# Kernel optimization log

Measured on AMD Instinct MI355X. Metric: run time of the kernel, lower is better.

## Reference

```python
import jax, jax.numpy as jnp
import numpy as np
import math

B, S, D, H = 2, 2048, 1024, 16
HD = D // H  # 64


def _rope(x, cos, sin):
    # x: [B,S,H,HD]; cos/sin: [S, HD//2]
    x2 = x.reshape(*x.shape[:-1], HD // 2, 2)
    x0, x1 = x2[..., 0], x2[..., 1]
    c = cos[None, :, None, :]
    s = sin[None, :, None, :]
    r0 = x0 * c - x1 * s
    r1 = x0 * s + x1 * c
    return jnp.stack([r0, r1], axis=-1).reshape(x.shape)


def setup_inputs() -> dict:
    key = jax.random.key(0)
    ks = jax.random.split(key, 6)
    x = jax.random.normal(ks[0], (B, S, D), dtype=jnp.float32)
    wq = jax.random.normal(ks[1], (D, D), dtype=jnp.float32) * 0.02
    wk = jax.random.normal(ks[2], (D, D), dtype=jnp.float32) * 0.02
    wv = jax.random.normal(ks[3], (D, D), dtype=jnp.float32) * 0.02
    wo = jax.random.normal(ks[4], (D, D), dtype=jnp.float32) * 0.02
    # standard RoPE frequencies: theta = 10000^(-2i/HD)
    inv_freq = 1.0 / (10000.0 ** (jnp.arange(0, HD, 2, dtype=jnp.float32) / HD))
    t = jnp.arange(S, dtype=jnp.float32)
    ang = t[:, None] * inv_freq[None, :]  # [S, HD//2]
    freqs_cos = jnp.cos(ang)
    freqs_sin = jnp.sin(ang)
    # causal additive mask [S, S]
    mask = jnp.where(jnp.tril(jnp.ones((S, S), dtype=bool)), 0.0, -1e9).astype(jnp.float32)
    return {"x": x, "wq": wq, "wk": wk, "wv": wv, "wo": wo,
            "freqs_cos": freqs_cos, "freqs_sin": freqs_sin, "mask": mask}


def reference(x, wq, wk, wv, wo, freqs_cos, freqs_sin, mask):
    b, s, d = x.shape
    # nn.Linear with no bias: y = x @ W^T
    q = jnp.einsum('bsd,od->bso', x, wq).reshape(b, s, H, HD)
    k = jnp.einsum('bsd,od->bso', x, wk).reshape(b, s, H, HD)
    v = jnp.einsum('bsd,od->bso', x, wv).reshape(b, s, H, HD)
    q = _rope(q, freqs_cos, freqs_sin)
    k = _rope(k, freqs_cos, freqs_sin)
    # [B,H,S,HD]
    q = q.transpose(0, 2, 1, 3)
    k = k.transpose(0, 2, 1, 3)
    v = v.transpose(0, 2, 1, 3)
    scores = jnp.einsum('bhqd,bhkd->bhqk', q, k) / math.sqrt(HD)
    scores = scores + mask[None, None, :, :]
    p = jax.nn.softmax(scores.astype(jnp.float32), axis=-1).astype(q.dtype)
    out = jnp.einsum('bhqk,bhkd->bhqd', p, v)
    out = out.transpose(0, 2, 1, 3).reshape(b, s, d)
    return jnp.einsum('bsd,od->bso', out, wo)
```

## Files before the change

kernel.cpp:

```cpp
#include <hip/hip_runtime.h>
#include <hip/hip_bf16.h>
#include <stdint.h>

#define NB 2
#define NS 2048
#define ND 1024
#define NH 16
#define NM (NB*NS)

typedef __attribute__((ext_vector_type(8))) short bf16x8;
typedef __attribute__((ext_vector_type(4))) float f32x4;

static __device__ __forceinline__ f32x4 mfma16(bf16x8 a, bf16x8 b, f32x4 c) {
  return __builtin_amdgcn_mfma_f32_16x16x32_bf16(a, b, c, 0, 0, 0);
}

static __device__ __forceinline__ void gload_lds16(const void* g, void* l) {
  __builtin_amdgcn_global_load_lds(
      (const __attribute__((address_space(1))) void*)g,
      (__attribute__((address_space(3))) void*)l, 16, 0, 0);
}

static __device__ __forceinline__ uint32_t pkbf2(float a, float b) {
  return (uint32_t)__bfloat16_as_ushort(__float2bfloat16(a)) |
         ((uint32_t)__bfloat16_as_ushort(__float2bfloat16(b)) << 16);
}

struct alignas(8) bh4 { __hip_bfloat16 x, y, z, w; };

__global__ void cvt_bf16(const float* __restrict__ in,
                         __hip_bfloat16* __restrict__ out, int n4) {
  int i = blockIdx.x * blockDim.x + threadIdx.x;
  int stride = gridDim.x * blockDim.x;
  for (; i < n4; i += stride) {
    float4 v = reinterpret_cast<const float4*>(in)[i];
    bh4 o;
    o.x = __float2bfloat16(v.x);
    o.y = __float2bfloat16(v.y);
    o.z = __float2bfloat16(v.z);
    o.w = __float2bfloat16(v.w);
    reinterpret_cast<bh4*>(out)[i] = o;
  }
}

__global__ void cvt_w4(const float* __restrict__ w0, const float* __restrict__ w1,
                       const float* __restrict__ w2, const float* __restrict__ w3,
                       __hip_bfloat16* o0, __hip_bfloat16* o1,
                       __hip_bfloat16* o2, __hip_bfloat16* o3) {
  const int t = blockIdx.x >> 10;
  const float* in = (t == 0) ? w0 : (t == 1) ? w1 : (t == 2) ? w2 : w3;
  __hip_bfloat16* out = (t == 0) ? o0 : (t == 1) ? o1 : (t == 2) ? o2 : o3;
  const int i = (blockIdx.x & 1023) * 256 + threadIdx.x;
  float4 v = reinterpret_cast<const float4*>(in)[i];
  bh4 o;
  o.x = __float2bfloat16(v.x);
  o.y = __float2bfloat16(v.y);
  o.z = __float2bfloat16(v.z);
  o.w = __float2bfloat16(v.w);
  reinterpret_cast<bh4*>(out)[i] = o;
}

template <int MODE>
__global__ __launch_bounds__(256) void gemm_proj(
    const __hip_bfloat16* __restrict__ A,
    const __hip_bfloat16* __restrict__ W,
    const float* __restrict__ fcos,
    const float* __restrict__ fsin,
    void* __restrict__ outp) {
  __shared__ __hip_bfloat16 sA[128 * 32];
  __shared__ __hip_bfloat16 sB[64 * 32];

  const int tid = threadIdx.x;
  const int wid = tid >> 6;
  const int lane = tid & 63;
  const int l4 = lane >> 4, l16 = lane & 15;
  const int brow = blockIdx.x * 128;
  const int bcol = blockIdx.y * 64;
  const int wr = (wid >> 1) * 64;
  const int wc = (wid & 1) * 32;

  f32x4 acc[4][2] = {};

  const __hip_bfloat16* Ap = A + (size_t)(brow + (tid >> 2)) * 1024 + (tid & 3) * 8;
  const __hip_bfloat16* Wp = W + (size_t)(bcol + (tid >> 2)) * 1024 + (tid & 3) * 8;
  char* sAc = (char*)sA + wid * 1024;
  char* sBc = (char*)sB + wid * 1024;

  for (int kt = 0; kt < 32; ++kt) {
    const int k0 = kt * 32;
    __syncthreads();
    gload_lds16(Ap + k0,             sAc);
    gload_lds16(Ap + 64 * 1024 + k0, sAc + 4096);
    gload_lds16(Wp + k0,             sBc);
    __syncthreads();

    bf16x8 af[4], bfr[2];
#pragma unroll
    for (int i = 0; i < 4; ++i)
      af[i] = *(const bf16x8*)&sA[(wr + i * 16 + l16) * 32 + l4 * 8];
#pragma unroll
    for (int i = 0; i < 2; ++i)
      bfr[i] = *(const bf16x8*)&sB[(wc + i * 16 + l16) * 32 + l4 * 8];
#pragma unroll
    for (int mi = 0; mi < 4; ++mi)
#pragma unroll
      for (int ni = 0; ni < 2; ++ni)
        acc[mi][ni] = mfma16(af[mi], bfr[ni], acc[mi][ni]);
  }

#pragma unroll
  for (int mi = 0; mi < 4; ++mi)
#pragma unroll
    for (int ni = 0; ni < 2; ++ni)
#pragma unroll
      for (int j = 0; j < 4; ++j) {
        float v = acc[mi][ni][j];
        const int row = brow + wr + mi * 16 + l4 * 4 + j;
        const int col = bcol + wc + ni * 16 + l16;
        if (MODE == 3) {
          ((float*)outp)[(size_t)row * 1024 + col] = v;
        } else if (MODE == 2) {
          const int bb = row >> 11, ss = row & 2047;
          const int hh = col >> 6, hd = col & 63;
          ((__hip_bfloat16*)outp)[((size_t)(bb * 16 + hh) * 64 + hd) * 2048 + ss] =
              __float2bfloat16(v);
        } else {
          float other = __shfl_xor(v, 1);
          const int ss = row & 2047;
          const int p = (col & 63) >> 1;
          const float c = fcos[ss * 32 + p];
          const float sn = fsin[ss * 32 + p];
          float r = (col & 1) ? (other * sn + v * c) : (v * c - other * sn);
          if (MODE == 0) r *= 0.125f;
          const int bb = row >> 11;
          const int hh = col >> 6, hd = col & 63;
          ((__hip_bfloat16*)outp)[((size_t)(bb * 16 + hh) * 2048 + ss) * 64 + hd] =
              __float2bfloat16(r);
        }
      }
}

__global__ __launch_bounds__(256) void attn_fwd(
    const __hip_bfloat16* __restrict__ Q,
    const __hip_bfloat16* __restrict__ K,
    const __hip_bfloat16* __restrict__ VT,
    __hip_bfloat16* __restrict__ AO) {
  const int L = blockIdx.x;
  int qt, bh;
  if (L < 256) { qt = 15 - (L >> 5); bh = L & 31; }
  else         { qt = (L >> 5) - 8;  bh = L & 31; }
  const int bb = bh >> 4;
  const int hh = bh & 15;
  const int tid = threadIdx.x;
  const int wid = tid >> 6;
  const int lane = tid & 63;
  const int l4 = lane >> 4, l16 = lane & 15;
  const int wq0 = qt * 128 + wid * 32;

  const __hip_bfloat16* Qg = Q + (size_t)bh * 2048 * 64;
  const __hip_bfloat16* Kg = K + (size_t)bh * 2048 * 64;
  const __hip_bfloat16* Vg = VT + (size_t)bh * 64 * 2048;

  __shared__ __hip_bfloat16 sK[2][64][72];
  __shared__ __hip_bfloat16 sV[2][64][72];
  __shared__ __hip_bfloat16 sP[4][32][72];

  bf16x8 qf[2][2];
#pragma unroll
  for (int q2 = 0; q2 < 2; ++q2)
#pragma unroll
    for (int dk = 0; dk < 2; ++dk)
      qf[q2][dk] = *(const bf16x8*)&Qg[(size_t)(wq0 + q2 * 16 + l16) * 64 + dk * 32 + l4 * 8];

  float mrun[2] = {-1e30f, -1e30f};
  float lrun[2] = {0.f, 0.f};
  f32x4 oacc[2][4] = {};

  const int sr = tid >> 3;
  const int so = (tid & 7) * 8;
  const int nkv = 2 * qt + 2;

  uint4 kreg[2], vreg[2];
#pragma unroll
  for (int i = 0; i < 2; ++i) {
    kreg[i] = *(const uint4*)&Kg[(size_t)(i * 32 + sr) * 64 + so];
    vreg[i] = *(const uint4*)&Vg[(size_t)(i * 32 + sr) * 2048 + so];
  }
#pragma unroll
  for (int i = 0; i < 2; ++i) {
    *(uint4*)&sK[0][i * 32 + sr][so] = kreg[i];
    *(uint4*)&sV[0][i * 32 + sr][so] = vreg[i];
  }
  __syncthreads();

  for (int kv = 0; kv < nkv; ++kv) {
    const int cur = kv & 1, nxt = cur ^ 1;
    const int kb = kv * 64;

    if (kv + 1 < nkv) {
      const int kb2 = kb + 64;
#pragma unroll
      for (int i = 0; i < 2; ++i) {
        kreg[i] = *(const uint4*)&Kg[(size_t)(kb2 + i * 32 + sr) * 64 + so];
        vreg[i] = *(const uint4*)&Vg[(size_t)(i * 32 + sr) * 2048 + kb2 + so];
      }
    }

    if (kb <= wq0 + 31) {
      f32x4 sacc[4][2] = {};
#pragma unroll
      for (int dk = 0; dk < 2; ++dk) {
        bf16x8 kfr[4];
#pragma unroll
        for (int kf = 0; kf < 4; ++kf)
          kfr[kf] = *(const bf16x8*)&sK[cur][kf * 16 + l16][dk * 32 + l4 * 8];
#pragma unroll
        for (int kf = 0; kf < 4; ++kf)
#pragma unroll
          for (int q2 = 0; q2 < 2; ++q2)
            sacc[kf][q2] = mfma16(kfr[kf], qf[q2][dk], sacc[kf][q2]);
      }

      const bool need_mask = (kb + 63 > wq0);
      float fac[2];
#pragma unroll
      for (int q2 = 0; q2 < 2; ++q2) {
        const int qi = wq0 + q2 * 16 + l16;
        float pv[16];
#pragma unroll
        for (int kf = 0; kf < 4; ++kf)
#pragma unroll
          for (int j = 0; j < 4; ++j) {
            float s = sacc[kf][q2][j];
            if (need_mask && (kb + kf * 16 + l4 * 4 + j > qi)) s = -1e30f;
            pv[kf * 4 + j] = s;
          }
        float m0 = fmaxf(fmaxf(pv[0], pv[1]), fmaxf(pv[2], pv[3]));
        float m1 = fmaxf(fmaxf(pv[4], pv[5]), fmaxf(pv[6], pv[7]));
        float m2 = fmaxf(fmaxf(pv[8], pv[9]), fmaxf(pv[10], pv[11]));
        float m3 = fmaxf(fmaxf(pv[12], pv[13]), fmaxf(pv[14], pv[15]));
        float mloc = fmaxf(fmaxf(m0, m1), fmaxf(m2, m3));
        mloc = fmaxf(mloc, __shfl_xor(mloc, 16));
        mloc = fmaxf(mloc, __shfl_xor(mloc, 32));
        const float mold = mrun[q2];
        const float mnew = fmaxf(mold, mloc);
        const float f = __expf(mold - mnew);
        fac[q2] = f;
        mrun[q2] = mnew;
        float ts = 0.f;
        float pe[16];
#pragma unroll
        for (int t = 0; t < 16; ++t) { pe[t] = __expf(pv[t] - mnew); ts += pe[t]; }
#pragma unroll
        for (int kf = 0; kf < 4; ++kf) {
          uint2 w;
          w.x = pkbf2(pe[kf * 4 + 0], pe[kf * 4 + 1]);
          w.y = pkbf2(pe[kf * 4 + 2], pe[kf * 4 + 3]);
          *(uint2*)&sP[wid][q2 * 16 + l16][kf * 16 + l4 * 4] = w;
        }
        ts += __shfl_xor(ts, 16);
        ts += __shfl_xor(ts, 32);
        lrun[q2] = lrun[q2] * f + ts;
      }

#pragma unroll
      for (int mf = 0; mf < 2; ++mf)
#pragma unroll
        for (int j = 0; j < 4; ++j) {
          const float fr = __shfl(fac[mf], l4 * 4 + j);
#pragma unroll
          for (int df = 0; df < 4; ++df) oacc[mf][df][j] *= fr;
        }

#pragma unroll
      for (int ks = 0; ks < 2; ++ks) {
        bf16x8 pfr[2], vfr[4];
#pragma unroll
        for (int mf = 0; mf < 2; ++mf)
          pfr[mf] = *(const bf16x8*)&sP[wid][mf * 16 + l16][ks * 32 + l4 * 8];
#pragma unroll
        for (int df = 0; df < 4; ++df)
          vfr[df] = *(const bf16x8*)&sV[cur][df * 16 + l16][ks * 32 + l4 * 8];
#pragma unroll
        for (int mf = 0; mf < 2; ++mf)
#pragma unroll
          for (int df = 0; df < 4; ++df)
            oacc[mf][df] = mfma16(pfr[mf], vfr[df], oacc[mf][df]);
      }
    }

    if (kv + 1 < nkv) {
#pragma unroll
      for (int i = 0; i < 2; ++i) {
        *(uint4*)&sK[nxt][i * 32 + sr][so] = kreg[i];
        *(uint4*)&sV[nxt][i * 32 + sr][so] = vreg[i];
      }
    }
    __syncthreads();
  }

  float inv[2];
#pragma unroll
  for (int q2 = 0; q2 < 2; ++q2) inv[q2] = 1.f / lrun[q2];
#pragma unroll
  for (int mf = 0; mf < 2; ++mf)
#pragma unroll
    for (int j = 0; j < 4; ++j) {
      const float ir = __shfl(inv[mf], l4 * 4 + j);
      const int ss = wq0 + mf * 16 + l4 * 4 + j;
#pragma unroll
      for (int df = 0; df < 4; ++df) {
        const int dd = hh * 64 + df * 16 + l16;
        AO[((size_t)bb * 2048 + ss) * 1024 + dd] =
            __float2bfloat16(oacc[mf][df][j] * ir);
      }
    }
}

extern "C" void kernel_launch(void* const* d_in, const int* in_sizes, int n_in,
                              void* d_out, int out_size, void* d_ws, size_t ws_size,
                              hipStream_t stream) {
  const float* x  = (const float*)d_in[0];
  const float* wq = (const float*)d_in[1];
  const float* wk = (const float*)d_in[2];
  const float* wv = (const float*)d_in[3];
  const float* wo = (const float*)d_in[4];
  const float* fc = (const float*)d_in[5];
  const float* fs = (const float*)d_in[6];

  char* ws = (char*)d_ws;
  const size_t MB = 1024 * 1024;
  __hip_bfloat16* xb  = (__hip_bfloat16*)(ws);
  __hip_bfloat16* wqb = (__hip_bfloat16*)(ws + 8 * MB);
  __hip_bfloat16* wkb = (__hip_bfloat16*)(ws + 10 * MB);
  __hip_bfloat16* wvb = (__hip_bfloat16*)(ws + 12 * MB);
  __hip_bfloat16* wob = (__hip_bfloat16*)(ws + 14 * MB);
  __hip_bfloat16* qws = (__hip_bfloat16*)(ws + 16 * MB);
  __hip_bfloat16* kws = (__hip_bfloat16*)(ws + 24 * MB);
  __hip_bfloat16* vws = (__hip_bfloat16*)(ws + 32 * MB);
  __hip_bfloat16* ao  = (__hip_bfloat16*)(ws + 40 * MB);

  cvt_bf16<<<2048, 256, 0, stream>>>(x, xb, NM * ND / 4);
  cvt_w4<<<4096, 256, 0, stream>>>(wq, wk, wv, wo, wqb, wkb, wvb, wob);

  dim3 g(NM / 128, ND / 64);
  gemm_proj<0><<<g, 256, 0, stream>>>(xb, wqb, fc, fs, (void*)qws);
  gemm_proj<1><<<g, 256, 0, stream>>>(xb, wkb, fc, fs, (void*)kws);
  gemm_proj<2><<<g, 256, 0, stream>>>(xb, wvb, fc, fs, (void*)vws);

  attn_fwd<<<dim3(512), 256, 0, stream>>>(qws, kws, vws, ao);

  gemm_proj<3><<<g, 256, 0, stream>>>(ao, wob, fc, fs, d_out);
}
```

Measured before the change: 268.7 us.

## Fuse QKV projections into one launch and stream K/V directly from global in attention

```diff
diff --git a/kernel.cpp b/kernel.cpp
--- a/kernel.cpp
+++ b/kernel.cpp
@@ -25,6 +25,8 @@
   return (uint32_t)__bfloat16_as_ushort(__float2bfloat16(a)) |
          ((uint32_t)__bfloat16_as_ushort(__float2bfloat16(b)) << 16);
 }
+
+#define QSCALE 0.18033688011112042f
 
 struct alignas(8) bh4 { __hip_bfloat16 x, y, z, w; };
 
@@ -60,13 +62,90 @@
   reinterpret_cast<bh4*>(out)[i] = o;
 }
 
-template <int MODE>
-__global__ __launch_bounds__(256) void gemm_proj(
+__global__ __launch_bounds__(256) void gemm_qkv(
+    const __hip_bfloat16* __restrict__ A,
+    const __hip_bfloat16* __restrict__ Wq,
+    const __hip_bfloat16* __restrict__ Wk,
+    const __hip_bfloat16* __restrict__ Wv,
+    const float* __restrict__ fcos,
+    const float* __restrict__ fsin,
+    __hip_bfloat16* __restrict__ Qo,
+    __hip_bfloat16* __restrict__ Ko,
+    __hip_bfloat16* __restrict__ Vo) {
+  __shared__ __hip_bfloat16 sA[128 * 32];
+  __shared__ __hip_bfloat16 sB[64 * 32];
+
+  const int wsel = blockIdx.y >> 4;
+  const __hip_bfloat16* W = (wsel == 0) ? Wq : (wsel == 1) ? Wk : Wv;
+
+  const int tid = threadIdx.x;
+  const int wid = tid >> 6;
+  const int lane = tid & 63;
+  const int l4 = lane >> 4, l16 = lane & 15;
+  const int brow = blockIdx.x * 128;
+  const int bcol = (blockIdx.y & 15) * 64;
+  const int wr = (wid >> 1) * 64;
+  const int wc = (wid & 1) * 32;
+
+  f32x4 acc[4][2] = {};
+
+  const __hip_bfloat16* Ap = A + (size_t)(brow + (tid >> 2)) * 1024 + (tid & 3) * 8;
+  const __hip_bfloat16* Wp = W + (size_t)(bcol + (tid >> 2)) * 1024 + (tid & 3) * 8;
+  char* sAc = (char*)sA + wid * 1024;
+  char* sBc = (char*)sB + wid * 1024;
+
+  for (int kt = 0; kt < 32; ++kt) {
+    const int k0 = kt * 32;
+    __syncthreads();
+    gload_lds16(Ap + k0,             sAc);
+    gload_lds16(Ap + 64 * 1024 + k0, sAc + 4096);
+    gload_lds16(Wp + k0,             sBc);
+    __syncthreads();
+
+    bf16x8 af[4], bfr[2];
+#pragma unroll
+    for (int i = 0; i < 4; ++i)
+      af[i] = *(const bf16x8*)&sA[(wr + i * 16 + l16) * 32 + l4 * 8];
+#pragma unroll
+    for (int i = 0; i < 2; ++i)
+      bfr[i] = *(const bf16x8*)&sB[(wc + i * 16 + l16) * 32 + l4 * 8];
+#pragma unroll
+    for (int mi = 0; mi < 4; ++mi)
+#pragma unroll
+      for (int ni = 0; ni < 2; ++ni)
+        acc[mi][ni] = mfma16(af[mi], bfr[ni], acc[mi][ni]);
+  }
+
+#pragma unroll
+  for (int mi = 0; mi < 4; ++mi)
+#pragma unroll
+    for (int ni = 0; ni < 2; ++ni)
+#pragma unroll
+      for (int j = 0; j < 4; ++j) {
+        float v = acc[mi][ni][j];
+        const int row = brow + wr + mi * 16 + l4 * 4 + j;
+        const int col = bcol + wc + ni * 16 + l16;
+        const int bb = row >> 11, ss = row & 2047;
+        const int hh = col >> 6, hd = col & 63;
+        if (wsel == 2) {
+          Vo[((size_t)(bb * 16 + hh) * 64 + hd) * 2048 + ss] = __float2bfloat16(v);
+        } else {
+          float other = __shfl_xor(v, 1);
+          const int p = hd >> 1;
+          const float c = fcos[ss * 32 + p];
+          const float sn = fsin[ss * 32 + p];
+          float r = (col & 1) ? (other * sn + v * c) : (v * c - other * sn);
+          __hip_bfloat16* dst = (wsel == 0) ? Qo : Ko;
+          if (wsel == 0) r *= QSCALE;
+          dst[((size_t)(bb * 16 + hh) * 2048 + ss) * 64 + hd] = __float2bfloat16(r);
+        }
+      }
+}
+
+__global__ __launch_bounds__(256) void gemm_out(
     const __hip_bfloat16* __restrict__ A,
     const __hip_bfloat16* __restrict__ W,
-    const float* __restrict__ fcos,
-    const float* __restrict__ fsin,
-    void* __restrict__ outp) {
+    float* __restrict__ C) {
   __shared__ __hip_bfloat16 sA[128 * 32];
   __shared__ __hip_bfloat16 sB[64 * 32];
 
@@ -114,29 +193,9 @@
     for (int ni = 0; ni < 2; ++ni)
 #pragma unroll
       for (int j = 0; j < 4; ++j) {
-        float v = acc[mi][ni][j];
         const int row = brow + wr + mi * 16 + l4 * 4 + j;
         const int col = bcol + wc + ni * 16 + l16;
-        if (MODE == 3) {
-          ((float*)outp)[(size_t)row * 1024 + col] = v;
-        } else if (MODE == 2) {
-          const int bb = row >> 11, ss = row & 2047;
-          const int hh = col >> 6, hd = col & 63;
-          ((__hip_bfloat16*)outp)[((size_t)(bb * 16 + hh) * 64 + hd) * 2048 + ss] =
-              __float2bfloat16(v);
-        } else {
-          float other = __shfl_xor(v, 1);
-          const int ss = row & 2047;
-          const int p = (col & 63) >> 1;
-          const float c = fcos[ss * 32 + p];
-          const float sn = fsin[ss * 32 + p];
-          float r = (col & 1) ? (other * sn + v * c) : (v * c - other * sn);
-          if (MODE == 0) r *= 0.125f;
-          const int bb = row >> 11;
-          const int hh = col >> 6, hd = col & 63;
-          ((__hip_bfloat16*)outp)[((size_t)(bb * 16 + hh) * 2048 + ss) * 64 + hd] =
-              __float2bfloat16(r);
-        }
+        C[(size_t)row * 1024 + col] = acc[mi][ni][j];
       }
 }
 
@@ -161,8 +220,6 @@
   const __hip_bfloat16* Kg = K + (size_t)bh * 2048 * 64;
   const __hip_bfloat16* Vg = VT + (size_t)bh * 64 * 2048;
 
-  __shared__ __hip_bfloat16 sK[2][64][72];
-  __shared__ __hip_bfloat16 sV[2][64][72];
   __shared__ __hip_bfloat16 sP[4][32][72];
 
   bf16x8 qf[2][2];
@@ -176,127 +233,96 @@
   float lrun[2] = {0.f, 0.f};
   f32x4 oacc[2][4] = {};
 
-  const int sr = tid >> 3;
-  const int so = (tid & 7) * 8;
-  const int nkv = 2 * qt + 2;
-
-  uint4 kreg[2], vreg[2];
-#pragma unroll
-  for (int i = 0; i < 2; ++i) {
-    kreg[i] = *(const uint4*)&Kg[(size_t)(i * 32 + sr) * 64 + so];
-    vreg[i] = *(const uint4*)&Vg[(size_t)(i * 32 + sr) * 2048 + so];
-  }
-#pragma unroll
-  for (int i = 0; i < 2; ++i) {
-    *(uint4*)&sK[0][i * 32 + sr][so] = kreg[i];
-    *(uint4*)&sV[0][i * 32 + sr][so] = vreg[i];
-  }
-  __syncthreads();
-
-  for (int kv = 0; kv < nkv; ++kv) {
-    const int cur = kv & 1, nxt = cur ^ 1;
+  const int lastkv = (wq0 + 31) >> 6;
+  for (int kv = 0; kv <= lastkv; ++kv) {
     const int kb = kv * 64;
 
-    if (kv + 1 < nkv) {
-      const int kb2 = kb + 64;
-#pragma unroll
-      for (int i = 0; i < 2; ++i) {
-        kreg[i] = *(const uint4*)&Kg[(size_t)(kb2 + i * 32 + sr) * 64 + so];
-        vreg[i] = *(const uint4*)&Vg[(size_t)(i * 32 + sr) * 2048 + kb2 + so];
-      }
+    bf16x8 kfr[4][2];
+#pragma unroll
+    for (int kf = 0; kf < 4; ++kf)
+#pragma unroll
+      for (int dk = 0; dk < 2; ++dk)
+        kfr[kf][dk] = *(const bf16x8*)&Kg[(size_t)(kb + kf * 16 + l16) * 64 + dk * 32 + l4 * 8];
+
+    f32x4 sacc[4][2] = {};
+#pragma unroll
+    for (int dk = 0; dk < 2; ++dk)
+#pragma unroll
+      for (int kf = 0; kf < 4; ++kf)
+#pragma unroll
+        for (int q2 = 0; q2 < 2; ++q2)
+          sacc[kf][q2] = mfma16(kfr[kf][dk], qf[q2][dk], sacc[kf][q2]);
+
+    bf16x8 vfr[4][2];
+#pragma unroll
+    for (int df = 0; df < 4; ++df)
+#pragma unroll
+      for (int ks = 0; ks < 2; ++ks)
+        vfr[df][ks] = *(const bf16x8*)&Vg[(size_t)(df * 16 + l16) * 2048 + kb + ks * 32 + l4 * 8];
+
+    const bool need_mask = (kb + 63 > wq0);
+    float fac[2];
+#pragma unroll
+    for (int q2 = 0; q2 < 2; ++q2) {
+      const int qi = wq0 + q2 * 16 + l16;
+      float pv[16];
+#pragma unroll
+      for (int kf = 0; kf < 4; ++kf)
+#pragma unroll
+        for (int j = 0; j < 4; ++j) {
+          float s = sacc[kf][q2][j];
+          if (need_mask && (kb + kf * 16 + l4 * 4 + j > qi)) s = -1e30f;
+          pv[kf * 4 + j] = s;
+        }
+      float m0 = fmaxf(fmaxf(pv[0], pv[1]), fmaxf(pv[2], pv[3]));
+      float m1 = fmaxf(fmaxf(pv[4], pv[5]), fmaxf(pv[6], pv[7]));
+      float m2 = fmaxf(fmaxf(pv[8], pv[9]), fmaxf(pv[10], pv[11]));
+      float m3 = fmaxf(fmaxf(pv[12], pv[13]), fmaxf(pv[14], pv[15]));
+      float mloc = fmaxf(fmaxf(m0, m1), fmaxf(m2, m3));
+      mloc = fmaxf(mloc, __shfl_xor(mloc, 16));
+      mloc = fmaxf(mloc, __shfl_xor(mloc, 32));
+      const float mold = mrun[q2];
+      const float mnew = fmaxf(mold, mloc);
+      const float f = exp2f(mold - mnew);
+      fac[q2] = f;
+      mrun[q2] = mnew;
+      float ts = 0.f;
+      float pe[16];
+#pragma unroll
+      for (int t = 0; t < 16; ++t) { pe[t] = exp2f(pv[t] - mnew); ts += pe[t]; }
+#pragma unroll
+      for (int kf = 0; kf < 4; ++kf) {
+        uint2 w;
+        w.x = pkbf2(pe[kf * 4 + 0], pe[kf * 4 + 1]);
+        w.y = pkbf2(pe[kf * 4 + 2], pe[kf * 4 + 3]);
+        *(uint2*)&sP[wid][q2 * 16 + l16][kf * 16 + l4 * 4] = w;
+      }
+      ts += __shfl_xor(ts, 16);
+      ts += __shfl_xor(ts, 32);
+      lrun[q2] = lrun[q2] * f + ts;
     }
 
-    if (kb <= wq0 + 31) {
-      f32x4 sacc[4][2] = {};
-#pragma unroll
-      for (int dk = 0; dk < 2; ++dk) {
-        bf16x8 kfr[4];
-#pragma unroll
-        for (int kf = 0; kf < 4; ++kf)
-          kfr[kf] = *(const bf16x8*)&sK[cur][kf * 16 + l16][dk * 32 + l4 * 8];
-#pragma unroll
-        for (int kf = 0; kf < 4; ++kf)
-#pragma unroll
-          for (int q2 = 0; q2 < 2; ++q2)
-            sacc[kf][q2] = mfma16(kfr[kf], qf[q2][dk], sacc[kf][q2]);
-      }
-
-      const bool need_mask = (kb + 63 > wq0);
-      float fac[2];
-#pragma unroll
-      for (int q2 = 0; q2 < 2; ++q2) {
-        const int qi = wq0 + q2 * 16 + l16;
-        float pv[16];
-#pragma unroll
-        for (int kf = 0; kf < 4; ++kf)
-#pragma unroll
-          for (int j = 0; j < 4; ++j) {
-            float s = sacc[kf][q2][j];
-            if (need_mask && (kb + kf * 16 + l4 * 4 + j > qi)) s = -1e30f;
-            pv[kf * 4 + j] = s;
-          }
-        float m0 = fmaxf(fmaxf(pv[0], pv[1]), fmaxf(pv[2], pv[3]));
-        float m1 = fmaxf(fmaxf(pv[4], pv[5]), fmaxf(pv[6], pv[7]));
-        float m2 = fmaxf(fmaxf(pv[8], pv[9]), fmaxf(pv[10], pv[11]));
-        float m3 = fmaxf(fmaxf(pv[12], pv[13]), fmaxf(pv[14], pv[15]));
-        float mloc = fmaxf(fmaxf(m0, m1), fmaxf(m2, m3));
-        mloc = fmaxf(mloc, __shfl_xor(mloc, 16));
-        mloc = fmaxf(mloc, __shfl_xor(mloc, 32));
-        const float mold = mrun[q2];
-        const float mnew = fmaxf(mold, mloc);
-        const float f = __expf(mold - mnew);
-        fac[q2] = f;
-        mrun[q2] = mnew;
-        float ts = 0.f;
-        float pe[16];
-#pragma unroll
-        for (int t = 0; t < 16; ++t) { pe[t] = __expf(pv[t] - mnew); ts += pe[t]; }
-#pragma unroll
-        for (int kf = 0; kf < 4; ++kf) {
-          uint2 w;
-          w.x = pkbf2(pe[kf * 4 + 0], pe[kf * 4 + 1]);
-          w.y = pkbf2(pe[kf * 4 + 2], pe[kf * 4 + 3]);
-          *(uint2*)&sP[wid][q2 * 16 + l16][kf * 16 + l4 * 4] = w;
-        }
-        ts += __shfl_xor(ts, 16);
-        ts += __shfl_xor(ts, 32);
-        lrun[q2] = lrun[q2] * f + ts;
-      }
-
+#pragma unroll
+    for (int mf = 0; mf < 2; ++mf)
+#pragma unroll
+      for (int j = 0; j < 4; ++j) {
+        const float fr = __shfl(fac[mf], l4 * 4 + j);
+#pragma unroll
+        for (int df = 0; df < 4; ++df) oacc[mf][df][j] *= fr;
+      }
+
+#pragma unroll
+    for (int ks = 0; ks < 2; ++ks) {
+      bf16x8 pfr[2];
 #pragma unroll
       for (int mf = 0; mf < 2; ++mf)
-#pragma unroll
-        for (int j = 0; j < 4; ++j) {
-          const float fr = __shfl(fac[mf], l4 * 4 + j);
-#pragma unroll
-          for (int df = 0; df < 4; ++df) oacc[mf][df][j] *= fr;
-        }
-
-#pragma unroll
-      for (int ks = 0; ks < 2; ++ks) {
-        bf16x8 pfr[2], vfr[4];
-#pragma unroll
-        for (int mf = 0; mf < 2; ++mf)
-          pfr[mf] = *(const bf16x8*)&sP[wid][mf * 16 + l16][ks * 32 + l4 * 8];
+        pfr[mf] = *(const bf16x8*)&sP[wid][mf * 16 + l16][ks * 32 + l4 * 8];
+#pragma unroll
+      for (int mf = 0; mf < 2; ++mf)
 #pragma unroll
         for (int df = 0; df < 4; ++df)
-          vfr[df] = *(const bf16x8*)&sV[cur][df * 16 + l16][ks * 32 + l4 * 8];
-#pragma unroll
-        for (int mf = 0; mf < 2; ++mf)
-#pragma unroll
-          for (int df = 0; df < 4; ++df)
-            oacc[mf][df] = mfma16(pfr[mf], vfr[df], oacc[mf][df]);
-      }
+          oacc[mf][df] = mfma16(pfr[mf], vfr[df][ks], oacc[mf][df]);
     }
-
-    if (kv + 1 < nkv) {
-#pragma unroll
-      for (int i = 0; i < 2; ++i) {
-        *(uint4*)&sK[nxt][i * 32 + sr][so] = kreg[i];
-        *(uint4*)&sV[nxt][i * 32 + sr][so] = vreg[i];
-      }
-    }
-    __syncthreads();
   }
 
   float inv[2];
@@ -343,12 +369,10 @@
   cvt_bf16<<<2048, 256, 0, stream>>>(x, xb, NM * ND / 4);
   cvt_w4<<<4096, 256, 0, stream>>>(wq, wk, wv, wo, wqb, wkb, wvb, wob);
 
-  dim3 g(NM / 128, ND / 64);
-  gemm_proj<0><<<g, 256, 0, stream>>>(xb, wqb, fc, fs, (void*)qws);
-  gemm_proj<1><<<g, 256, 0, stream>>>(xb, wkb, fc, fs, (void*)kws);
-  gemm_proj<2><<<g, 256, 0, stream>>>(xb, wvb, fc, fs, (void*)vws);
+  gemm_qkv<<<dim3(NM / 128, 48), 256, 0, stream>>>(xb, wqb, wkb, wvb, fc, fs,
+                                                   qws, kws, vws);
 
   attn_fwd<<<dim3(512), 256, 0, stream>>>(qws, kws, vws, ao);
 
-  gemm_proj<3><<<g, 256, 0, stream>>>(ao, wob, fc, fs, d_out);
-}
+  gemm_out<<<dim3(NM / 128, ND / 64), 256, 0, stream>>>(ao, wob, (float*)d_out);
+}
```

New measurement: 246.5 us. 1.09x faster.
